# Performance work log

Measured on AMD Instinct MI355X. Metric: run time of the kernel, lower is better.

## Reference

```python
import jax, jax.numpy as jnp
import numpy as np

# Irreps structure: (multiplicity, component dim 2l+1) for 64x0e + 32x1o + 16x2e
MULTS = (64, 32, 16)
DIMS = (1, 3, 5)
N_NODES = 65536
NUM_TYPES = 64


def setup_inputs() -> dict:
    key = jax.random.key(0)
    k_x, k_idx, k0, k1, k2 = jax.random.split(key, 5)
    dim = sum(m * d for m, d in zip(MULTS, DIMS))  # 240
    x = jax.random.normal(k_x, (N_NODES, dim), dtype=jnp.float32)
    idx = jax.random.randint(k_idx, (N_NODES,), 0, NUM_TYPES)
    W0 = jax.random.normal(k0, (NUM_TYPES, 64, 64), dtype=jnp.float32)
    W1 = jax.random.normal(k1, (NUM_TYPES, 32, 32), dtype=jnp.float32)
    W2 = jax.random.normal(k2, (NUM_TYPES, 16, 16), dtype=jnp.float32)
    return {"x": x, "W0": W0, "W1": W1, "W2": W2, "idx": idx}


def reference(x, W0, W1, W2, idx):
    """Indexed e3nn-style linear: per-node index gathers a weight set; each
    irrep block mixes multiplicity channels (shared across the 2l+1 components)
    with e3nn path normalization 1/sqrt(m_in)."""
    n = x.shape[0]
    outs = []
    off = 0
    for W, m, d in zip((W0, W1, W2), MULTS, DIMS):
        blk = x[:, off:off + m * d].reshape(n, m, d)  # [N, m_in, 2l+1]
        off += m * d
        Wn = W[idx]  # gather per-node weights: [N, m_in, m_out]
        scale = np.float32(1.0 / np.sqrt(m))
        out = jnp.einsum('nio,nid->nod', Wn, blk) * scale  # [N, m_out, 2l+1]
        outs.append(out.reshape(n, m * d))
    return jnp.concatenate(outs, axis=-1)
```

## Files before the change

### kernel.cpp

```cpp
#include <hip/hip_runtime.h>

typedef __attribute__((ext_vector_type(8))) short short8;
typedef __attribute__((ext_vector_type(4))) float floatx4;

#define NTYPES    64
#define WT_STRIDE 5632
#define WROWS     16
#define ROW_U     248
#define CPAD      16

__device__ __forceinline__ unsigned short f2bf(float f) {
    union { float f; unsigned u; } v; v.f = f;
    unsigned u = v.u;
    u += 0x7FFFu + ((u >> 16) & 1u);
    return (unsigned short)(u >> 16);
}

__global__ __launch_bounds__(256) void wt_kernel(const float* __restrict__ W0,
                                                 const float* __restrict__ W1,
                                                 const float* __restrict__ W2,
                                                 unsigned short* __restrict__ wt,
                                                 int* __restrict__ gcount) {
    __shared__ float ws0[4096];
    __shared__ float ws1[1024];
    __shared__ float ws2[256];
    const int t = blockIdx.x, tid = threadIdx.x;
    if (t == 0 && tid < NTYPES) gcount[tid * CPAD] = 0;
    const float4* s0 = (const float4*)(W0 + (size_t)t * 4096);
#pragma unroll
    for (int j = 0; j < 4; ++j) ((float4*)ws0)[j * 256 + tid] = s0[j * 256 + tid];
    ((float4*)ws1)[tid] = ((const float4*)(W1 + (size_t)t * 1024))[tid];
    if (tid < 64) ((float4*)ws2)[tid] = ((const float4*)(W2 + (size_t)t * 256))[tid];
    __syncthreads();
    unsigned short* dst = wt + (size_t)t * WT_STRIDE;
    for (int e = tid; e < 4096; e += 256) {
        int f = e >> 9, rem = e & 511, rr = rem >> 5, k2 = rem & 31;
        int i = (f & 1) * 32 + k2, o = (f >> 1) * 16 + rr;
        dst[e] = f2bf(ws0[i * 64 + o] * 0.125f);
    }
    for (int e = tid; e < 1024; e += 256) {
        int h = e >> 9, rem = e & 511, rr = rem >> 5, k = rem & 31;
        dst[4096 + e] = f2bf(ws1[k * 32 + h * 16 + rr] * 0.17677669529663687f);
    }
    for (int e = tid; e < 512; e += 256) {
        int rr = e >> 5, k = e & 31;
        dst[5120 + e] = (k < 16) ? f2bf(ws2[k * 16 + rr] * 0.25f) : (unsigned short)0;
    }
}

__global__ __launch_bounds__(256) void hist_kernel(const int* __restrict__ idx,
                                                   int* __restrict__ gcount, int n) {
    __shared__ int c[NTYPES];
    const int tid = threadIdx.x, g = blockIdx.x * 256 + tid;
    if (tid < NTYPES) c[tid] = 0;
    __syncthreads();
    if (g < n) atomicAdd(&c[idx[g]], 1);
    __syncthreads();
    if (tid < NTYPES && c[tid]) atomicAdd(&gcount[tid * CPAD], c[tid]);
}

__global__ __launch_bounds__(64) void base_kernel(const int* __restrict__ gcount,
                                                  int* __restrict__ gcur) {
    const int t = threadIdx.x;
    int v = gcount[t * CPAD];
    int s = v;
#pragma unroll
    for (int o = 1; o < 64; o <<= 1) {
        int u = __shfl_up(s, o);
        if (t >= o) s += u;
    }
    gcur[t * CPAD] = s - v;
}

__global__ __launch_bounds__(256) void scatter_kernel(const int* __restrict__ idx,
                                                      int* __restrict__ gcur,
                                                      int* __restrict__ psort, int n) {
    __shared__ int c[NTYPES], off[NTYPES], cur[NTYPES];
    const int tid = threadIdx.x, g = blockIdx.x * 256 + tid;
    if (tid < NTYPES) { c[tid] = 0; cur[tid] = 0; }
    __syncthreads();
    int ty = -1;
    if (g < n) { ty = idx[g]; atomicAdd(&c[ty], 1); }
    __syncthreads();
    if (tid < NTYPES && c[tid]) off[tid] = atomicAdd(&gcur[tid * CPAD], c[tid]);
    __syncthreads();
    if (g < n) {
        int rk = atomicAdd(&cur[ty], 1);
        psort[off[ty] + rk] = g | (ty << 24);
    }
}

__global__ __launch_bounds__(64, 4) void main_kernel(
    const float* __restrict__ x,
    const int* __restrict__ psort,
    const unsigned short* __restrict__ wt,
    float* __restrict__ out, int n)
{
    __shared__ __align__(16) unsigned short xrow[WROWS * ROW_U];

    const int b = blockIdx.x, ln = threadIdx.x;
    const int nbase = b * WROWS;
    const int nv = min(WROWS, n - nbase);

    int pl = 0;
    if (ln < WROWS && (nbase + ln) < n) pl = psort[nbase + ln];

#pragma unroll
    for (int it = 0; it < 15; ++it) {
        int e = it * 64 + ln;
        int row = e / 60, c4 = e - row * 60;
        int prow = __shfl(pl, row);
        if (row < nv) {
            int node = prow & 0xFFFFFF;
            float4 f = *(const float4*)(x + (size_t)node * 240 + c4 * 4);
            unsigned short qq[4] = {f2bf(f.x), f2bf(f.y), f2bf(f.z), f2bf(f.w)};
            unsigned short* xr = xrow + row * ROW_U;
            if (c4 < 16) {
                *(ushort4*)(xr + c4 * 4) = ushort4{qq[0], qq[1], qq[2], qq[3]};
            } else if (c4 < 40) {
                int t0 = c4 * 4 - 64;
                int i = t0 / 3, d = t0 - i * 3;
#pragma unroll
                for (int j = 0; j < 4; ++j) {
                    xr[64 + d * 32 + i] = qq[j];
                    if (++d == 3) { d = 0; ++i; }
                }
            } else {
                int t0 = c4 * 4 - 160;
                int i = t0 / 5, d = t0 - i * 5;
#pragma unroll
                for (int j = 0; j < 4; ++j) {
                    xr[160 + d * 16 + i] = qq[j];
                    if (++d == 5) { d = 0; ++i; }
                }
            }
        }
    }
    __syncthreads();

    const int r = ln & 15, q4 = ln >> 4;

    const unsigned short* xr = xrow + min(r, nv - 1) * ROW_U;
    short8 bx0 = *(const short8*)(xr + q4 * 8);
    short8 bx1 = *(const short8*)(xr + 32 + q4 * 8);
    short8 b1d[3];
#pragma unroll
    for (int d = 0; d < 3; ++d) b1d[d] = *(const short8*)(xr + 64 + d * 32 + q4 * 8);
    short8 b2d[5];
#pragma unroll
    for (int d = 0; d < 5; ++d) b2d[d] = *(const short8*)(xr + 160 + d * 16 + (q4 & 1) * 8);

    const int prow_r = __shfl(pl, r);
    const bool vrow = (r < nv);
    float* op = out + (size_t)(prow_r & 0xFFFFFF) * 240;

    int ti  = __shfl(pl, r) >> 24;
    int tim = __shfl(pl, (r > 0) ? (r - 1) : 0) >> 24;
    bool bnd = (r == 0) || (ti != tim);
    unsigned m = (unsigned)(__ballot(bnd) & 0xFFFFull);

    while (m) {
        const int slo = __builtin_ctz(m);
        const unsigned m2 = m & (m - 1u);
        const int shi = m2 ? __builtin_ctz(m2) : nv;
        const int tyseg = __shfl(pl, slo) >> 24;
        const unsigned short* wb = wt + (size_t)tyseg * WT_STRIDE;
        const bool vst = vrow && (r >= slo) && (r < shi);

#pragma unroll
        for (int nt = 0; nt < 4; ++nt) {
            short8 wa = *(const short8*)(wb + (nt * 2) * 512 + r * 32 + q4 * 8);
            short8 wc = *(const short8*)(wb + (nt * 2 + 1) * 512 + r * 32 + q4 * 8);
            floatx4 ac = {0.f, 0.f, 0.f, 0.f};
            ac = __builtin_amdgcn_mfma_f32_16x16x32_bf16(wa, bx0, ac, 0, 0, 0);
            ac = __builtin_amdgcn_mfma_f32_16x16x32_bf16(wc, bx1, ac, 0, 0, 0);
            if (vst) *(floatx4*)(op + nt * 16 + q4 * 4) = ac;
        }

        {
            short8 wc0 = *(const short8*)(wb + 4096 + r * 32 + q4 * 8);
            short8 wc1 = *(const short8*)(wb + 4096 + 512 + r * 32 + q4 * 8);
            floatx4 a1[2][3];
#pragma unroll
            for (int d = 0; d < 3; ++d) {
                floatx4 z = {0.f, 0.f, 0.f, 0.f};
                a1[0][d] = __builtin_amdgcn_mfma_f32_16x16x32_bf16(wc0, b1d[d], z, 0, 0, 0);
                a1[1][d] = __builtin_amdgcn_mfma_f32_16x16x32_bf16(wc1, b1d[d], z, 0, 0, 0);
            }
            if (vst) {
#pragma unroll
                for (int h = 0; h < 2; ++h) {
                    float* o1 = op + 64 + (h * 16 + q4 * 4) * 3;
                    floatx4 v0 = {a1[h][0][0], a1[h][1][0], a1[h][2][0], a1[h][0][1]};
                    floatx4 v1 = {a1[h][1][1], a1[h][2][1], a1[h][0][2], a1[h][1][2]};
                    floatx4 v2 = {a1[h][2][2], a1[h][0][3], a1[h][1][3], a1[h][2][3]};
                    *(floatx4*)(o1)     = v0;
                    *(floatx4*)(o1 + 4) = v1;
                    *(floatx4*)(o1 + 8) = v2;
                }
            }
        }

        {
            short8 wc2 = *(const short8*)(wb + 5120 + r * 32 + q4 * 8);
            floatx4 a2[5];
#pragma unroll
            for (int d = 0; d < 5; ++d) {
                floatx4 z = {0.f, 0.f, 0.f, 0.f};
                a2[d] = __builtin_amdgcn_mfma_f32_16x16x32_bf16(wc2, b2d[d], z, 0, 0, 0);
            }
            if (vst) {
                float* o2 = op + 160 + q4 * 20;
                floatx4 v0 = {a2[0][0], a2[1][0], a2[2][0], a2[3][0]};
                floatx4 v1 = {a2[4][0], a2[0][1], a2[1][1], a2[2][1]};
                floatx4 v2 = {a2[3][1], a2[4][1], a2[0][2], a2[1][2]};
                floatx4 v3 = {a2[2][2], a2[3][2], a2[4][2], a2[0][3]};
                floatx4 v4 = {a2[1][3], a2[2][3], a2[3][3], a2[4][3]};
                *(floatx4*)(o2)      = v0;
                *(floatx4*)(o2 + 4)  = v1;
                *(floatx4*)(o2 + 8)  = v2;
                *(floatx4*)(o2 + 12) = v3;
                *(floatx4*)(o2 + 16) = v4;
            }
        }
        m = m2;
    }
}

extern "C" void kernel_launch(void* const* d_in, const int* in_sizes, int n_in,
                              void* d_out, int out_size, void* d_ws, size_t ws_size,
                              hipStream_t stream) {
    const float* x  = (const float*)d_in[0];
    const float* W0 = (const float*)d_in[1];
    const float* W1 = (const float*)d_in[2];
    const float* W2 = (const float*)d_in[3];
    const int*   idx = (const int*)d_in[4];
    float* out = (float*)d_out;
    const int n = in_sizes[4];
    const int nb = (n + 255) / 256;

    char* ws = (char*)d_ws;
    unsigned short* wt = (unsigned short*)ws;
    size_t off = (size_t)NTYPES * WT_STRIDE * 2;
    int* psort  = (int*)(ws + off); off += (size_t)n * 4;
    int* gcount = (int*)(ws + off); off += (size_t)NTYPES * CPAD * 4;
    int* gcur   = (int*)(ws + off);

    wt_kernel     <<<NTYPES, 256, 0, stream>>>(W0, W1, W2, wt, gcount);
    hist_kernel   <<<nb, 256, 0, stream>>>(idx, gcount, n);
    base_kernel   <<<1, 64, 0, stream>>>(gcount, gcur);
    scatter_kernel<<<nb, 256, 0, stream>>>(idx, gcur, psort, n);
    main_kernel   <<<(n + WROWS - 1) / WROWS, 64, 0, stream>>>(x, psort, wt, out, n);
}
```

Baseline: 150.0 us.

## Load x fragments directly into registers, drop LDS staging, pack 4 waves per block

The main kernel no longer stages gathered node rows through shared memory with scalar transposing stores. Each lane now loads its MFMA B-fragment floats straight from global memory and converts them with packed bf16 conversion instructions, so the l=1 and l=2 component transposes happen in registers. Blocks grow from one wave to four independent waves, each handling 16 sorted nodes. This removes the LDS round trip, the scattered 2-byte stores and the block barrier. In exchange, overlapping lanes issue redundant global loads of the same x elements and register pressure rises.

```diff
diff --git a/kernel.cpp b/kernel.cpp
--- a/kernel.cpp
+++ b/kernel.cpp
@@ -2,11 +2,11 @@
 
 typedef __attribute__((ext_vector_type(8))) short short8;
 typedef __attribute__((ext_vector_type(4))) float floatx4;
+typedef __attribute__((ext_vector_type(4))) unsigned uintx4;
 
 #define NTYPES    64
 #define WT_STRIDE 5632
 #define WROWS     16
-#define ROW_U     248
 #define CPAD      16
 
 __device__ __forceinline__ unsigned short f2bf(float f) {
@@ -14,6 +14,12 @@
     unsigned u = v.u;
     u += 0x7FFFu + ((u >> 16) & 1u);
     return (unsigned short)(u >> 16);
+}
+
+__device__ __forceinline__ unsigned pk2(float lo, float hi) {
+    unsigned r;
+    asm("v_cvt_pk_bf16_f32 %0, %1, %2" : "=v"(r) : "v"(lo), "v"(hi));
+    return r;
 }
 
 __global__ __launch_bounds__(256) void wt_kernel(const float* __restrict__ W0,
@@ -90,69 +96,65 @@
     }
 }
 
-__global__ __launch_bounds__(64, 4) void main_kernel(
+__global__ __launch_bounds__(256, 4) void main_kernel(
     const float* __restrict__ x,
     const int* __restrict__ psort,
     const unsigned short* __restrict__ wt,
     float* __restrict__ out, int n)
 {
-    __shared__ __align__(16) unsigned short xrow[WROWS * ROW_U];
-
-    const int b = blockIdx.x, ln = threadIdx.x;
-    const int nbase = b * WROWS;
+    const int tid = threadIdx.x, wv = tid >> 6, ln = tid & 63;
+    const int w = blockIdx.x * 4 + wv;
+    const int nbase = w * WROWS;
+    if (nbase >= n) return;
     const int nv = min(WROWS, n - nbase);
 
     int pl = 0;
     if (ln < WROWS && (nbase + ln) < n) pl = psort[nbase + ln];
 
-#pragma unroll
-    for (int it = 0; it < 15; ++it) {
-        int e = it * 64 + ln;
-        int row = e / 60, c4 = e - row * 60;
-        int prow = __shfl(pl, row);
-        if (row < nv) {
-            int node = prow & 0xFFFFFF;
-            float4 f = *(const float4*)(x + (size_t)node * 240 + c4 * 4);
-            unsigned short qq[4] = {f2bf(f.x), f2bf(f.y), f2bf(f.z), f2bf(f.w)};
-            unsigned short* xr = xrow + row * ROW_U;
-            if (c4 < 16) {
-                *(ushort4*)(xr + c4 * 4) = ushort4{qq[0], qq[1], qq[2], qq[3]};
-            } else if (c4 < 40) {
-                int t0 = c4 * 4 - 64;
-                int i = t0 / 3, d = t0 - i * 3;
-#pragma unroll
-                for (int j = 0; j < 4; ++j) {
-                    xr[64 + d * 32 + i] = qq[j];
-                    if (++d == 3) { d = 0; ++i; }
-                }
-            } else {
-                int t0 = c4 * 4 - 160;
-                int i = t0 / 5, d = t0 - i * 5;
-#pragma unroll
-                for (int j = 0; j < 4; ++j) {
-                    xr[160 + d * 16 + i] = qq[j];
-                    if (++d == 5) { d = 0; ++i; }
-                }
-            }
-        }
-    }
-    __syncthreads();
-
     const int r = ln & 15, q4 = ln >> 4;
-
-    const unsigned short* xr = xrow + min(r, nv - 1) * ROW_U;
-    short8 bx0 = *(const short8*)(xr + q4 * 8);
-    short8 bx1 = *(const short8*)(xr + 32 + q4 * 8);
-    short8 b1d[3];
-#pragma unroll
-    for (int d = 0; d < 3; ++d) b1d[d] = *(const short8*)(xr + 64 + d * 32 + q4 * 8);
-    short8 b2d[5];
-#pragma unroll
-    for (int d = 0; d < 5; ++d) b2d[d] = *(const short8*)(xr + 160 + d * 16 + (q4 & 1) * 8);
-
-    const int prow_r = __shfl(pl, r);
+    const int prow = __shfl(pl, min(r, nv - 1));
+    const int node = prow & 0xFFFFFF;
+    const float* xp = x + (size_t)node * 240;
+
+    union frag { short8 s; uintx4 u; };
+
+    float4 f0a = *(const float4*)(xp + q4 * 8);
+    float4 f0b = *(const float4*)(xp + q4 * 8 + 4);
+    float4 f0c = *(const float4*)(xp + 32 + q4 * 8);
+    float4 f0d = *(const float4*)(xp + 32 + q4 * 8 + 4);
+    frag bx0, bx1;
+    bx0.u = uintx4{pk2(f0a.x, f0a.y), pk2(f0a.z, f0a.w),
+                   pk2(f0b.x, f0b.y), pk2(f0b.z, f0b.w)};
+    bx1.u = uintx4{pk2(f0c.x, f0c.y), pk2(f0c.z, f0c.w),
+                   pk2(f0d.x, f0d.y), pk2(f0d.z, f0d.w)};
+
+    const float4* xg = (const float4*)(xp + 64 + q4 * 24);
+    float4 g0 = xg[0], g1 = xg[1], g2 = xg[2], g3 = xg[3], g4 = xg[4], g5 = xg[5];
+    const float G[24] = {g0.x, g0.y, g0.z, g0.w, g1.x, g1.y, g1.z, g1.w,
+                         g2.x, g2.y, g2.z, g2.w, g3.x, g3.y, g3.z, g3.w,
+                         g4.x, g4.y, g4.z, g4.w, g5.x, g5.y, g5.z, g5.w};
+    frag b1d[3];
+#pragma unroll
+    for (int d = 0; d < 3; ++d)
+        b1d[d].u = uintx4{pk2(G[d], G[3 + d]), pk2(G[6 + d], G[9 + d]),
+                          pk2(G[12 + d], G[15 + d]), pk2(G[18 + d], G[21 + d])};
+
+    const float4* xh = (const float4*)(xp + 160 + (q4 & 1) * 40);
+    float4 h0 = xh[0], h1 = xh[1], h2 = xh[2], h3 = xh[3], h4 = xh[4];
+    float4 h5 = xh[5], h6 = xh[6], h7 = xh[7], h8 = xh[8], h9 = xh[9];
+    const float H[40] = {h0.x, h0.y, h0.z, h0.w, h1.x, h1.y, h1.z, h1.w,
+                         h2.x, h2.y, h2.z, h2.w, h3.x, h3.y, h3.z, h3.w,
+                         h4.x, h4.y, h4.z, h4.w, h5.x, h5.y, h5.z, h5.w,
+                         h6.x, h6.y, h6.z, h6.w, h7.x, h7.y, h7.z, h7.w,
+                         h8.x, h8.y, h8.z, h8.w, h9.x, h9.y, h9.z, h9.w};
+    frag b2d[5];
+#pragma unroll
+    for (int d = 0; d < 5; ++d)
+        b2d[d].u = uintx4{pk2(H[d], H[5 + d]), pk2(H[10 + d], H[15 + d]),
+                          pk2(H[20 + d], H[25 + d]), pk2(H[30 + d], H[35 + d])};
+
     const bool vrow = (r < nv);
-    float* op = out + (size_t)(prow_r & 0xFFFFFF) * 240;
+    float* op = out + (size_t)node * 240;
 
     int ti  = __shfl(pl, r) >> 24;
     int tim = __shfl(pl, (r > 0) ? (r - 1) : 0) >> 24;
@@ -172,8 +174,8 @@
             short8 wa = *(const short8*)(wb + (nt * 2) * 512 + r * 32 + q4 * 8);
             short8 wc = *(const short8*)(wb + (nt * 2 + 1) * 512 + r * 32 + q4 * 8);
             floatx4 ac = {0.f, 0.f, 0.f, 0.f};
-            ac = __builtin_amdgcn_mfma_f32_16x16x32_bf16(wa, bx0, ac, 0, 0, 0);
-            ac = __builtin_amdgcn_mfma_f32_16x16x32_bf16(wc, bx1, ac, 0, 0, 0);
+            ac = __builtin_amdgcn_mfma_f32_16x16x32_bf16(wa, bx0.s, ac, 0, 0, 0);
+            ac = __builtin_amdgcn_mfma_f32_16x16x32_bf16(wc, bx1.s, ac, 0, 0, 0);
             if (vst) *(floatx4*)(op + nt * 16 + q4 * 4) = ac;
         }
 
@@ -184,8 +186,8 @@
 #pragma unroll
             for (int d = 0; d < 3; ++d) {
                 floatx4 z = {0.f, 0.f, 0.f, 0.f};
-                a1[0][d] = __builtin_amdgcn_mfma_f32_16x16x32_bf16(wc0, b1d[d], z, 0, 0, 0);
-                a1[1][d] = __builtin_amdgcn_mfma_f32_16x16x32_bf16(wc1, b1d[d], z, 0, 0, 0);
+                a1[0][d] = __builtin_amdgcn_mfma_f32_16x16x32_bf16(wc0, b1d[d].s, z, 0, 0, 0);
+                a1[1][d] = __builtin_amdgcn_mfma_f32_16x16x32_bf16(wc1, b1d[d].s, z, 0, 0, 0);
             }
             if (vst) {
 #pragma unroll
@@ -207,7 +209,7 @@
 #pragma unroll
             for (int d = 0; d < 5; ++d) {
                 floatx4 z = {0.f, 0.f, 0.f, 0.f};
-                a2[d] = __builtin_amdgcn_mfma_f32_16x16x32_bf16(wc2, b2d[d], z, 0, 0, 0);
+                a2[d] = __builtin_amdgcn_mfma_f32_16x16x32_bf16(wc2, b2d[d].s, z, 0, 0, 0);
             }
             if (vst) {
                 float* o2 = op + 160 + q4 * 20;
@@ -250,5 +252,5 @@
     hist_kernel   <<<nb, 256, 0, stream>>>(idx, gcount, n);
     base_kernel   <<<1, 64, 0, stream>>>(gcount, gcur);
     scatter_kernel<<<nb, 256, 0, stream>>>(idx, gcur, psort, n);
-    main_kernel   <<<(n + WROWS - 1) / WROWS, 64, 0, stream>>>(x, psort, wt, out, n);
-}
+    main_kernel   <<<(n + 4 * WROWS - 1) / (4 * WROWS), 256, 0, stream>>>(x, psort, wt, out, n);
+}
```

Result: no change. 150.7 us (+0.4%).
